# Optimization experiments

Measured on AMD Instinct MI355X. Metric: run time of the kernel, lower is better.

Reference implementation:

```python
import jax, jax.numpy as jnp
import numpy as np

B, S, D, U = 16, 1024, 1024, 512  # batch, seq, d_model, cfc_units
LN_EPS = 1e-5


def setup_inputs() -> dict:
    key = jax.random.key(0)
    ks = jax.random.split(key, 12)
    sd_in = 1.0 / np.sqrt(D)
    sd_u = 1.0 / np.sqrt(U)
    return {
        "x": jax.random.normal(ks[0], (B, S, D), dtype=jnp.float32),
        "ln_gamma": jnp.ones((D,), jnp.float32),
        "ln_beta": jnp.zeros((D,), jnp.float32),
        # input_proj: Linear(D -> U)
        "w_in": jax.random.uniform(ks[1], (U, D), jnp.float32, -sd_in, sd_in),
        "b_in": jax.random.uniform(ks[2], (U,), jnp.float32, -sd_in, sd_in),
        # GRU weights (PyTorch layout: [3U, U], gate order r, z, n)
        "w_ih": jax.random.uniform(ks[3], (3 * U, U), jnp.float32, -sd_u, sd_u),
        "w_hh": jax.random.uniform(ks[4], (3 * U, U), jnp.float32, -sd_u, sd_u),
        "b_ih": jax.random.uniform(ks[5], (3 * U,), jnp.float32, -sd_u, sd_u),
        "b_hh": jax.random.uniform(ks[6], (3 * U,), jnp.float32, -sd_u, sd_u),
        # output_proj: Linear(U -> D)
        "w_out": jax.random.uniform(ks[7], (D, U), jnp.float32, -sd_u, sd_u),
        "b_out": jax.random.uniform(ks[8], (D,), jnp.float32, -sd_u, sd_u),
    }


def _layernorm(x, gamma, beta):
    mu = jnp.mean(x, axis=-1, keepdims=True)
    var = jnp.mean(jnp.square(x - mu), axis=-1, keepdims=True)
    return (x - mu) * jax.lax.rsqrt(var + LN_EPS) * gamma + beta


def reference(x, ln_gamma, ln_beta, w_in, b_in, w_ih, w_hh, b_ih, b_hh, w_out, b_out):
    residual = x
    xn = _layernorm(x, ln_gamma, ln_beta)                       # [B,S,D]
    u = jnp.einsum("bsd,ud->bsu", xn, w_in) + b_in              # [B,S,U]
    # precompute input-side gate activations for all timesteps (one big GEMM)
    gx = jnp.einsum("bsu,gu->bsg", u, w_ih) + b_ih              # [B,S,3U]

    def step(h, gx_t):                                          # gx_t [B,3U]
        gh = h @ w_hh.T + b_hh                                  # [B,3U]
        xr, xz, xn_ = jnp.split(gx_t, 3, axis=-1)
        hr, hz, hn = jnp.split(gh, 3, axis=-1)
        r = jax.nn.sigmoid(xr + hr)
        z = jax.nn.sigmoid(xz + hz)
        n = jnp.tanh(xn_ + r * hn)
        h_new = (1.0 - z) * n + z * h
        return h_new, h_new

    h0 = jnp.zeros((x.shape[0], w_hh.shape[1]), dtype=jnp.float32)
    h_last, ys = jax.lax.scan(step, h0, jnp.swapaxes(gx, 0, 1))  # ys [S,B,U]
    y = jnp.swapaxes(ys, 0, 1)                                   # [B,S,U]
    out = residual + (jnp.einsum("bsu,du->bsd", y, w_out) + b_out)
    return out, h_last
```

## Files before the change

### kernel.cpp

```cpp
#include <hip/hip_runtime.h>

typedef unsigned short ushort_t;
typedef unsigned int uint_t;
typedef __attribute__((ext_vector_type(8))) short bf16x8;
typedef __attribute__((ext_vector_type(4))) float f32x4;
typedef __attribute__((ext_vector_type(4))) unsigned int uintx4;

#define B_  16
#define S_  1024
#define D_  1024
#define U_  512
#define GU_ 1536

__device__ __forceinline__ ushort_t f2bf(float f) {
  union { float f; uint_t u; } v; v.f = f;
  uint_t r = v.u + 0x7fffu + ((v.u >> 16) & 1u);
  return (ushort_t)(r >> 16);
}
__device__ __forceinline__ float bf2f(ushort_t b) {
  union { uint_t u; float f; } v; v.u = ((uint_t)b) << 16; return v.f;
}

__global__ void cvt_f32_bf16(const float4* __restrict__ in, ushort4* __restrict__ out, int n4) {
  int i = blockIdx.x * blockDim.x + threadIdx.x;
  int stride = gridDim.x * blockDim.x;
  for (; i < n4; i += stride) {
    float4 f = in[i];
    ushort4 o; o.x = f2bf(f.x); o.y = f2bf(f.y); o.z = f2bf(f.z); o.w = f2bf(f.w);
    out[i] = o;
  }
}

__global__ __launch_bounds__(256) void ln_kernel(
    const float* __restrict__ x, const float* __restrict__ gamma,
    const float* __restrict__ beta, ushort_t* __restrict__ xn)
{
  int row = blockIdx.x;
  int t = threadIdx.x;
  const float* xr = x + (size_t)row * 1024;
  float4 v = *(const float4*)(xr + t * 4);
  float s = v.x + v.y + v.z + v.w;
  float ss = v.x * v.x + v.y * v.y + v.z * v.z + v.w * v.w;
#pragma unroll
  for (int o = 32; o > 0; o >>= 1) {
    s  += __shfl_down(s, o, 64);
    ss += __shfl_down(ss, o, 64);
  }
  __shared__ float red[2][4];
  __shared__ float mv[2];
  int wv = t >> 6, ln = t & 63;
  if (ln == 0) { red[0][wv] = s; red[1][wv] = ss; }
  __syncthreads();
  if (t == 0) {
    float S1 = red[0][0] + red[0][1] + red[0][2] + red[0][3];
    float S2 = red[1][0] + red[1][1] + red[1][2] + red[1][3];
    float mu = S1 * (1.f / 1024.f);
    float var = S2 * (1.f / 1024.f) - mu * mu;
    mv[0] = mu;
    mv[1] = rsqrtf(var + 1e-5f);
  }
  __syncthreads();
  float mu = mv[0], rs = mv[1];
  float4 gm = *(const float4*)(gamma + t * 4);
  float4 bt = *(const float4*)(beta + t * 4);
  ushort4 o;
  o.x = f2bf((v.x - mu) * rs * gm.x + bt.x);
  o.y = f2bf((v.y - mu) * rs * gm.y + bt.y);
  o.z = f2bf((v.z - mu) * rs * gm.z + bt.z);
  o.w = f2bf((v.w - mu) * rs * gm.w + bt.w);
  *(ushort4*)(xn + (size_t)row * 1024 + t * 4) = o;
}

template<int RES, int OBF>
__global__ __launch_bounds__(256, 2) void gemm_bt(
    const ushort_t* __restrict__ A, const ushort_t* __restrict__ Bw,
    const float* __restrict__ bias, const float* __restrict__ resid,
    void* __restrict__ Cout, int M, int N, int K)
{
  __shared__ ushort_t As[128][40];
  __shared__ ushort_t Bs[128][40];
  int bm = blockIdx.x, bn = blockIdx.y;
  int tid = threadIdx.x;
  int wave = tid >> 6, lane = tid & 63;
  int wm = wave >> 1, wn = wave & 1;
  int q = lane >> 4, l16 = lane & 15;
  f32x4 acc[4][4];
#pragma unroll
  for (int i = 0; i < 4; i++)
#pragma unroll
    for (int j = 0; j < 4; j++) acc[i][j] = (f32x4){0.f, 0.f, 0.f, 0.f};
  int r0 = tid >> 2, kc = tid & 3;
  const int nk = K >> 5;
  for (int it = 0; it < nk; ++it) {
#pragma unroll
    for (int h = 0; h < 2; ++h) {
      int r = r0 + h * 64;
      const uint4* pa = (const uint4*)(A + (size_t)(bm * 128 + r) * K + it * 32 + kc * 8);
      *(uint4*)&As[r][kc * 8] = *pa;
      const uint4* pb = (const uint4*)(Bw + (size_t)(bn * 128 + r) * K + it * 32 + kc * 8);
      *(uint4*)&Bs[r][kc * 8] = *pb;
    }
    __syncthreads();
    bf16x8 af[4], bfr[4];
#pragma unroll
    for (int i = 0; i < 4; i++) af[i]  = *(bf16x8*)&As[wm * 64 + i * 16 + l16][q * 8];
#pragma unroll
    for (int j = 0; j < 4; j++) bfr[j] = *(bf16x8*)&Bs[wn * 64 + j * 16 + l16][q * 8];
#pragma unroll
    for (int i = 0; i < 4; i++)
#pragma unroll
      for (int j = 0; j < 4; j++)
        acc[i][j] = __builtin_amdgcn_mfma_f32_16x16x32_bf16(af[i], bfr[j], acc[i][j], 0, 0, 0);
    __syncthreads();
  }
#pragma unroll
  for (int i = 0; i < 4; i++) {
#pragma unroll
    for (int j = 0; j < 4; j++) {
      int n = bn * 128 + wn * 64 + j * 16 + l16;
      float bv = bias[n];
#pragma unroll
      for (int rr = 0; rr < 4; rr++) {
        int m = bm * 128 + wm * 64 + i * 16 + q * 4 + rr;
        float v = acc[i][j][rr] + bv;
        if (RES) v += resid[(size_t)m * N + n];
        if (OBF) ((ushort_t*)Cout)[(size_t)m * N + n] = f2bf(v);
        else     ((float*)Cout)[(size_t)m * N + n] = v;
      }
    }
  }
}

__global__ __launch_bounds__(128, 1) void scan_kernel(
    const ushort_t* __restrict__ gx, const float* __restrict__ w_hh,
    const float* __restrict__ b_hh, uint_t* __restrict__ mdata,
    uint_t* __restrict__ mtag, ushort_t* __restrict__ y,
    float* __restrict__ h_last)
{
  extern __shared__ char smem[];
  ushort_t* wlds = (ushort_t*)smem;
  char* hshb = smem + 49152;

  const int m = blockIdx.x;
  const int c0 = m * 32;
  const int t = threadIdx.x;
  const int wv = t >> 6, lane = t & 63, q = lane >> 4, l16 = lane & 15;
  const int cl = (wv << 4) + l16;

  for (int idx = t; idx < 48 * 64; idx += 128) {
    int cc = idx >> 6, ln = idx & 63;
    int gi = cc >> 4, wv2 = (cc >> 3) & 1, ks = cc & 7;
    int n = c0 + (wv2 << 4) + (ln & 15);
    int k0 = (ks << 5) + ((ln >> 4) << 3);
    const float* src = w_hh + (size_t)(gi * 512 + n) * 512 + k0;
    float4 f0 = *(const float4*)src;
    float4 f1 = *(const float4*)(src + 4);
    uint4 pk;
    pk.x = (uint_t)f2bf(f0.x) | ((uint_t)f2bf(f0.y) << 16);
    pk.y = (uint_t)f2bf(f0.z) | ((uint_t)f2bf(f0.w) << 16);
    pk.z = (uint_t)f2bf(f1.x) | ((uint_t)f2bf(f1.y) << 16);
    pk.w = (uint_t)f2bf(f1.z) | ((uint_t)f2bf(f1.w) << 16);
    *(uint4*)(wlds + (size_t)cc * 512 + ln * 8) = pk;
  }
  bf16x8 wreg[3][8];
#pragma unroll
  for (int gi = 0; gi < 3; ++gi)
#pragma unroll
    for (int k8 = 0; k8 < 8; ++k8) {
      const float* src = w_hh + (size_t)(gi * 512 + c0 + cl) * 512 + (8 + k8) * 32 + q * 8;
      float4 f0 = *(const float4*)src;
      float4 f1 = *(const float4*)(src + 4);
      bf16x8 wf;
      wf[0] = (short)f2bf(f0.x); wf[1] = (short)f2bf(f0.y);
      wf[2] = (short)f2bf(f0.z); wf[3] = (short)f2bf(f0.w);
      wf[4] = (short)f2bf(f1.x); wf[5] = (short)f2bf(f1.y);
      wf[6] = (short)f2bf(f1.z); wf[7] = (short)f2bf(f1.w);
      wreg[gi][k8] = wf;
    }

  const float bhr = b_hh[c0 + cl];
  const float bhz = b_hh[512 + c0 + cl];
  const float bhn = b_hh[1024 + c0 + cl];
  float hcur[4] = {0.f, 0.f, 0.f, 0.f};

  ushort_t gxv[3][4];
#pragma unroll
  for (int g = 0; g < 3; ++g)
#pragma unroll
    for (int r = 0; r < 4; ++r)
      gxv[g][r] = gx[(size_t)(((q << 2) + r) * S_) * GU_ + g * 512 + c0 + cl];

  for (int i = t; i < 4096; i += 128) ((uint_t*)hshb)[i] = 0u;

  const int l64 = t & 63;
  for (int step = 0; step < S_; ++step) {
    if (step > 0) {
      const uint_t want = (uint_t)step;
      const int slot = (step - 1) & 1;
      const uint_t* tp = mtag + slot * 16 + (lane & 15);
      uint_t tv;
      do {
        asm volatile("global_load_dword %0, %1, off sc0 sc1"
                     : "=v"(tv) : "v"(tp) : "memory");
        asm volatile("s_waitcnt vmcnt(0)" ::: "memory");
      } while (!__all((int)(tv == want)));
      const uint_t* db = mdata + slot * 4096;
      uintx4 vals[8];
#pragma unroll
      for (int j = 0; j < 8; ++j) {
        const uint_t* p = db + j * 512 + t * 4;
        asm volatile("global_load_dwordx4 %0, %1, off sc0 sc1"
                     : "=v"(vals[j]) : "v"(p) : "memory");
      }
      asm volatile("s_waitcnt vmcnt(0)" ::: "memory");
#pragma unroll
      for (int j = 0; j < 8; ++j) {
        int b = 2 * j + wv;
        *(uint4*)(hshb + b * 1024 + ((l64 ^ (b & 7)) << 4)) = *(uint4*)&vals[j];
      }
    }
    __syncthreads();

    f32x4 acc[3] = {{0.f,0.f,0.f,0.f},{0.f,0.f,0.f,0.f},{0.f,0.f,0.f,0.f}};
#pragma unroll
    for (int ks = 0; ks < 16; ++ks) {
      bf16x8 hf = *(bf16x8*)(hshb + l16 * 1024 +
                             ((((ks << 2) + q) ^ (l16 & 7)) << 4));
#pragma unroll
      for (int gi = 0; gi < 3; ++gi) {
        bf16x8 wf;
        if (ks < 8) wf = *(bf16x8*)(wlds + (size_t)((gi * 2 + wv) * 8 + ks) * 512 + lane * 8);
        else        wf = wreg[gi][ks - 8];
        acc[gi] = __builtin_amdgcn_mfma_f32_16x16x32_bf16(hf, wf, acc[gi], 0, 0, 0);
      }
    }

    ushort_t hb16[4];
#pragma unroll
    for (int r = 0; r < 4; ++r) {
      float xr  = bf2f(gxv[0][r]);
      float xz  = bf2f(gxv[1][r]);
      float xnn = bf2f(gxv[2][r]);
      float rr = 1.f / (1.f + __expf(-(xr + acc[0][r] + bhr)));
      float zz = 1.f / (1.f + __expf(-(xz + acc[1][r] + bhz)));
      float na = xnn + rr * (acc[2][r] + bhn);
      float ng = 1.f - 2.f / (1.f + __expf(2.f * na));
      float hv = (1.f - zz) * ng + zz * hcur[r];
      hcur[r] = hv;
      hb16[r] = f2bf(hv);
    }

    if (step < S_ - 1) {
      const int oslot = step & 1;
#pragma unroll
      for (int r = 0; r < 4; ++r) {
        uint_t other = (uint_t)__shfl_xor((int)(uint_t)hb16[r], 1, 64);
        if ((lane & 1) == 0) {
          uint_t dw = ((uint_t)hb16[r]) | (other << 16);
          int b = (q << 2) + r;
          uint_t* pp = mdata + oslot * 4096 + b * 256 + ((c0 + cl) >> 1);
          asm volatile("global_store_dword %0, %1, off sc0 sc1"
                       :: "v"(pp), "v"(dw) : "memory");
        }
      }
      __syncthreads();
      if (t == 0) {
        uint_t tagv = (uint_t)(step + 1);
        uint_t* tp = mtag + oslot * 16 + m;
        asm volatile("global_store_dword %0, %1, off sc0 sc1"
                     :: "v"(tp), "v"(tagv) : "memory");
      }
    }

#pragma unroll
    for (int r = 0; r < 4; ++r)
      y[((size_t)((q << 2) + r) * S_ + step) * U_ + c0 + cl] = hb16[r];

    if (step + 1 < S_) {
#pragma unroll
      for (int g = 0; g < 3; ++g)
#pragma unroll
        for (int r = 0; r < 4; ++r)
          gxv[g][r] = gx[((size_t)((q << 2) + r) * S_ + step + 1) * GU_ +
                         g * 512 + c0 + cl];
    }
  }

#pragma unroll
  for (int r = 0; r < 4; ++r)
    h_last[((q << 2) + r) * 512 + c0 + cl] = hcur[r];
}

extern "C" void kernel_launch(void* const* d_in, const int* in_sizes, int n_in,
                              void* d_out, int out_size, void* d_ws, size_t ws_size,
                              hipStream_t stream) {
  const float* x     = (const float*)d_in[0];
  const float* ln_g  = (const float*)d_in[1];
  const float* ln_b  = (const float*)d_in[2];
  const float* w_in  = (const float*)d_in[3];
  const float* b_in  = (const float*)d_in[4];
  const float* w_ih  = (const float*)d_in[5];
  const float* w_hh  = (const float*)d_in[6];
  const float* b_ih  = (const float*)d_in[7];
  const float* b_hh  = (const float*)d_in[8];
  const float* w_out = (const float*)d_in[9];
  const float* b_out = (const float*)d_in[10];

  float* out = (float*)d_out;
  float* h_last = out + (size_t)B_ * S_ * D_;

  char* ws = (char*)d_ws;
  size_t off = 0;
  ushort_t* xn   = (ushort_t*)(ws + off); off += (size_t)B_ * S_ * D_ * 2;
  ushort_t* u    = (ushort_t*)(ws + off); off += (size_t)B_ * S_ * U_ * 2;
  ushort_t* gx   = (ushort_t*)(ws + off); off += (size_t)B_ * S_ * GU_ * 2;
  ushort_t* y    = (ushort_t*)(ws + off); off += (size_t)B_ * S_ * U_ * 2;
  ushort_t* winb = (ushort_t*)(ws + off); off += (size_t)U_ * D_ * 2;
  ushort_t* wihb = (ushort_t*)(ws + off); off += (size_t)GU_ * U_ * 2;
  ushort_t* woub = (ushort_t*)(ws + off); off += (size_t)D_ * U_ * 2;
  uint_t* mtag   = (uint_t*)(ws + off);   off += 256;
  uint_t* mdata  = (uint_t*)xn;

  cvt_f32_bf16<<<512, 256, 0, stream>>>((const float4*)w_in,  (ushort4*)winb, U_ * D_ / 4);
  cvt_f32_bf16<<<512, 256, 0, stream>>>((const float4*)w_ih,  (ushort4*)wihb, GU_ * U_ / 4);
  cvt_f32_bf16<<<512, 256, 0, stream>>>((const float4*)w_out, (ushort4*)woub, D_ * U_ / 4);

  ln_kernel<<<B_ * S_, 256, 0, stream>>>(x, ln_g, ln_b, xn);

  gemm_bt<0, 1><<<dim3(B_ * S_ / 128, U_ / 128), 256, 0, stream>>>(
      xn, winb, b_in, nullptr, u, B_ * S_, U_, D_);
  gemm_bt<0, 1><<<dim3(B_ * S_ / 128, GU_ / 128), 256, 0, stream>>>(
      u, wihb, b_ih, nullptr, gx, B_ * S_, GU_, U_);

  hipMemsetAsync(mtag, 0, 256, stream);

  (void)hipFuncSetAttribute(reinterpret_cast<const void*>(scan_kernel),
                            hipFuncAttributeMaxDynamicSharedMemorySize, 65536);
  scan_kernel<<<16, 128, 65536, stream>>>(gx, w_hh, b_hh, mdata, mtag, y, h_last);

  gemm_bt<1, 0><<<dim3(B_ * S_ / 128, D_ / 128), 256, 0, stream>>>(
      y, woub, b_out, x, out, B_ * S_, D_, U_);
}
```

Measured before the change: 3.083 ms.

## Embed step tags in exchanged hidden-state words to remove separate flag handshake

The cross-block hidden-state exchange in the scan kernel now packs each bf16 hidden value with a 16-bit step tag in one 32-bit word. Consumers poll the data buffer directly until every tag matches the step. This removes the separate tag array, the block-wide barrier before publishing the tag, and the extra round trip of tag-then-data loads. The cost is twice the exchange traffic per step and a heavier poll loop that reloads the full buffer, plus reliance on the xn workspace being free of stale values matching the tag pattern.

```diff
diff --git a/kernel.cpp b/kernel.cpp
--- a/kernel.cpp
+++ b/kernel.cpp
@@ -134,8 +134,7 @@
 __global__ __launch_bounds__(128, 1) void scan_kernel(
     const ushort_t* __restrict__ gx, const float* __restrict__ w_hh,
     const float* __restrict__ b_hh, uint_t* __restrict__ mdata,
-    uint_t* __restrict__ mtag, ushort_t* __restrict__ y,
-    float* __restrict__ h_last)
+    ushort_t* __restrict__ y, float* __restrict__ h_last)
 {
   extern __shared__ char smem[];
   ushort_t* wlds = (ushort_t*)smem;
@@ -192,31 +191,34 @@
 
   for (int i = t; i < 4096; i += 128) ((uint_t*)hshb)[i] = 0u;
 
-  const int l64 = t & 63;
   for (int step = 0; step < S_; ++step) {
     if (step > 0) {
       const uint_t want = (uint_t)step;
-      const int slot = (step - 1) & 1;
-      const uint_t* tp = mtag + slot * 16 + (lane & 15);
-      uint_t tv;
-      do {
-        asm volatile("global_load_dword %0, %1, off sc0 sc1"
-                     : "=v"(tv) : "v"(tp) : "memory");
+      const uint_t* db = mdata + (((step - 1) & 1) << 13);
+      uintx4 vals[16];
+      for (;;) {
+#pragma unroll
+        for (int j = 0; j < 16; ++j) {
+          const uint_t* p = db + j * 512 + t * 4;
+          asm volatile("global_load_dwordx4 %0, %1, off sc0 sc1"
+                       : "=v"(vals[j]) : "v"(p) : "memory");
+        }
         asm volatile("s_waitcnt vmcnt(0)" ::: "memory");
-      } while (!__all((int)(tv == want)));
-      const uint_t* db = mdata + slot * 4096;
-      uintx4 vals[8];
-#pragma unroll
-      for (int j = 0; j < 8; ++j) {
-        const uint_t* p = db + j * 512 + t * 4;
-        asm volatile("global_load_dwordx4 %0, %1, off sc0 sc1"
-                     : "=v"(vals[j]) : "v"(p) : "memory");
-      }
-      asm volatile("s_waitcnt vmcnt(0)" ::: "memory");
-#pragma unroll
-      for (int j = 0; j < 8; ++j) {
-        int b = 2 * j + wv;
-        *(uint4*)(hshb + b * 1024 + ((l64 ^ (b & 7)) << 4)) = *(uint4*)&vals[j];
+        uint_t bad = 0u;
+#pragma unroll
+        for (int j = 0; j < 16; ++j) {
+          uintx4 v = vals[j];
+          bad |= ((v.x ^ want) | (v.y ^ want) | (v.z ^ want) | (v.w ^ want)) & 0xffffu;
+        }
+        if (!__any((int)bad)) break;
+      }
+#pragma unroll
+      for (int j = 0; j < 16; ++j) {
+        uintx4 v = vals[j];
+        uint2 dw;
+        dw.x = (v.x >> 16) | (v.y & 0xffff0000u);
+        dw.y = (v.z >> 16) | (v.w & 0xffff0000u);
+        *(uint2*)(hshb + j * 1024 + (((t >> 1) ^ (j & 7)) << 4) + ((t & 1) << 3)) = dw;
       }
     }
     __syncthreads();
@@ -251,24 +253,14 @@
     }
 
     if (step < S_ - 1) {
-      const int oslot = step & 1;
+      const uint_t tagout = (uint_t)(step + 1);
+      uint_t* pb = mdata + ((step & 1) << 13);
 #pragma unroll
       for (int r = 0; r < 4; ++r) {
-        uint_t other = (uint_t)__shfl_xor((int)(uint_t)hb16[r], 1, 64);
-        if ((lane & 1) == 0) {
-          uint_t dw = ((uint_t)hb16[r]) | (other << 16);
-          int b = (q << 2) + r;
-          uint_t* pp = mdata + oslot * 4096 + b * 256 + ((c0 + cl) >> 1);
-          asm volatile("global_store_dword %0, %1, off sc0 sc1"
-                       :: "v"(pp), "v"(dw) : "memory");
-        }
-      }
-      __syncthreads();
-      if (t == 0) {
-        uint_t tagv = (uint_t)(step + 1);
-        uint_t* tp = mtag + oslot * 16 + m;
+        uint_t dw = (((uint_t)hb16[r]) << 16) | tagout;
+        uint_t* pp = pb + ((q << 2) + r) * 512 + c0 + cl;
         asm volatile("global_store_dword %0, %1, off sc0 sc1"
-                     :: "v"(tp), "v"(tagv) : "memory");
+                     :: "v"(pp), "v"(dw) : "memory");
       }
     }
 
@@ -284,6 +276,8 @@
           gxv[g][r] = gx[((size_t)((q << 2) + r) * S_ + step + 1) * GU_ +
                          g * 512 + c0 + cl];
     }
+
+    asm volatile("s_barrier" ::: "memory");
   }
 
 #pragma unroll
@@ -318,7 +312,6 @@
   ushort_t* winb = (ushort_t*)(ws + off); off += (size_t)U_ * D_ * 2;
   ushort_t* wihb = (ushort_t*)(ws + off); off += (size_t)GU_ * U_ * 2;
   ushort_t* woub = (ushort_t*)(ws + off); off += (size_t)D_ * U_ * 2;
-  uint_t* mtag   = (uint_t*)(ws + off);   off += 256;
   uint_t* mdata  = (uint_t*)xn;
 
   cvt_f32_bf16<<<512, 256, 0, stream>>>((const float4*)w_in,  (ushort4*)winb, U_ * D_ / 4);
@@ -332,11 +325,9 @@
   gemm_bt<0, 1><<<dim3(B_ * S_ / 128, GU_ / 128), 256, 0, stream>>>(
       u, wihb, b_ih, nullptr, gx, B_ * S_, GU_, U_);
 
-  hipMemsetAsync(mtag, 0, 256, stream);
-
   (void)hipFuncSetAttribute(reinterpret_cast<const void*>(scan_kernel),
                             hipFuncAttributeMaxDynamicSharedMemorySize, 65536);
-  scan_kernel<<<16, 128, 65536, stream>>>(gx, w_hh, b_hh, mdata, mtag, y, h_last);
+  scan_kernel<<<16, 128, 65536, stream>>>(gx, w_hh, b_hh, mdata, y, h_last);
 
   gemm_bt<1, 0><<<dim3(B_ * S_ / 128, D_ / 128), 256, 0, stream>>>(
       y, woub, b_out, x, out, B_ * S_, D_, U_);
```

After: 3.169 ms. 1.03x slower.
